# Kernel optimization log

Measured on AMD Instinct MI355X. Metric: run time of the kernel, lower is better.

Reference implementation:

```python
import jax, jax.numpy as jnp
import numpy as np

EPS = 1e-5

def _fake_quant(w, axis):
    # symmetric int8 fake-quant with straight-through estimator
    s = jnp.max(jnp.abs(w), axis=axis, keepdims=True) / 127.0 + 1e-8
    q = jnp.clip(jnp.round(w / s), -127.0, 127.0) * s
    return w + jax.lax.stop_gradient(q - w)

def _qconv1x1(x, w, b):
    # x: [B, C_in, Q, H, W]; w: [C_out, C_in] (1x1 kernel); weight fake-quantized
    wq = _fake_quant(w, axis=1)
    return jnp.einsum('bcqhw,oc->boqhw', x, wq) + b[None, :, None, None, None]

def setup_inputs() -> dict:
    key = jax.random.key(0)
    ks = jax.random.split(key, 12)
    B, C, Q, H, W = 8, 256, 4, 40, 40
    x = jax.random.normal(ks[0], (B, C, Q, H, W), dtype=jnp.float32)
    scale = 1.0 / np.sqrt(C)
    Wq = jax.random.normal(ks[1], (C, C), dtype=jnp.float32) * scale
    Wk = jax.random.normal(ks[2], (C, C), dtype=jnp.float32) * scale
    Wv = jax.random.normal(ks[3], (C, C), dtype=jnp.float32) * scale
    Wp = jax.random.normal(ks[4], (C, C), dtype=jnp.float32) * scale
    bq = jnp.zeros((C,), jnp.float32)
    bk = jnp.zeros((C,), jnp.float32)
    bv = jnp.zeros((C,), jnp.float32)
    bp = jnp.zeros((C,), jnp.float32)
    gamma = jnp.ones((C,), jnp.float32)
    beta = jnp.zeros((C,), jnp.float32)
    return {"x": x, "Wq": Wq, "bq": bq, "Wk": Wk, "bk": bk,
            "Wv": Wv, "bv": bv, "Wp": Wp, "bp": bp,
            "gamma": gamma, "beta": beta}

def reference(x, Wq, bq, Wk, bk, Wv, bv, Wp, bp, gamma, beta):
    B, C, Q, H, W = x.shape
    q = _qconv1x1(x, Wq, bq)
    k = _qconv1x1(x, Wk, bk)
    v = _qconv1x1(x, Wv, bv)
    # per-rotation channel attention: [B, Q=4, C, H*W]
    qh = q.reshape(B, C, Q, H * W).transpose(0, 2, 1, 3)
    kh = k.reshape(B, C, Q, H * W).transpose(0, 2, 1, 3)
    vh = v.reshape(B, C, Q, H * W).transpose(0, 2, 1, 3)
    scale = 1.0 / jnp.sqrt(jnp.float32(C // 4))
    attn = jnp.einsum('bqcn,bqdn->bqcd', qh, kh) * scale  # [B,4,C,C]
    attn = jax.nn.softmax(attn, axis=-1)
    out = jnp.einsum('bqcd,bqdn->bqcn', attn, vh)  # [B,4,C,HW]
    out = out.transpose(0, 2, 1, 3).reshape(B, C, Q, H, W)
    out = _qconv1x1(out, Wp, bp)
    # IQBN: per-channel batchnorm with int8 fake-quantized gamma
    mean = jnp.mean(out, axis=(0, 2, 3, 4), keepdims=True)
    var = jnp.var(out, axis=(0, 2, 3, 4), keepdims=True)
    g = _fake_quant(gamma, axis=None)[None, :, None, None, None]
    b = beta[None, :, None, None, None]
    out = (out - mean) * jax.lax.rsqrt(var + EPS) * g + b
    return out
```

## Files before the change

### kernel.cpp

```cpp
#include <hip/hip_runtime.h>
#include <math.h>

#define BB 8
#define CCH 256
#define QQ 4
#define NN 1600
#define BQN 32
#define SP 51200
#define EPSF 1e-5f

typedef __attribute__((ext_vector_type(8))) short bf16x8;
typedef __attribute__((ext_vector_type(4))) float f32x4;

static __device__ inline ushort f2bf(float f) {
  union { float f; unsigned u; } v; v.f = f;
  return (ushort)((v.u + 0x7fffu + ((v.u >> 16) & 1u)) >> 16);
}
static __device__ inline float bf2f(ushort u) {
  union { unsigned u; float f; } v; v.u = ((unsigned)u) << 16;
  return v.f;
}
static __device__ inline void gld16(const ushort* g, ushort* l) {
  __builtin_amdgcn_global_load_lds(
      (const __attribute__((address_space(1))) unsigned int*)g,
      (__attribute__((address_space(3))) unsigned int*)l, 16, 0, 0);
}

__global__ void quant_weights_kernel(const float* Wq, const float* Wk,
                                     const float* Wv, const float* Wp,
                                     const float* gamma,
                                     ushort* wq, ushort* wk, ushort* wvT, ushort* wp,
                                     ushort* wqT, ushort* wkT, ushort* wpT,
                                     float* gq, float* r, float* d2,
                                     float* m_acc, float* v_acc) {
  __shared__ float red[256];
  int blk = blockIdx.x;
  int tid = threadIdx.x;
  if (blk < 1024) {
    int mat = blk >> 8;
    int row = blk & 255;
    const float* W = (mat == 0) ? Wq : (mat == 1) ? Wk : (mat == 2) ? Wv : Wp;
    float w = W[row * 256 + tid];
    red[tid] = fabsf(w);
    __syncthreads();
    for (int s = 128; s > 0; s >>= 1) {
      if (tid < s) red[tid] = fmaxf(red[tid], red[tid + s]);
      __syncthreads();
    }
    float s = red[0] / 127.0f + 1e-8f;
    float q = fminf(fmaxf(rintf(w / s), -127.0f), 127.0f) * s;
    ushort qb = f2bf(q);
    if (mat == 0)      { wq[row * 256 + tid] = qb; wqT[tid * 256 + row] = qb; }
    else if (mat == 1) { wk[row * 256 + tid] = qb; wkT[tid * 256 + row] = qb; }
    else if (mat == 2) { wvT[tid * 256 + row] = qb; }
    else               { wp[row * 256 + tid] = qb; wpT[tid * 256 + row] = qb; }
  } else {
    float g = gamma[tid];
    red[tid] = fabsf(g);
    __syncthreads();
    for (int s = 128; s > 0; s >>= 1) {
      if (tid < s) red[tid] = fmaxf(red[tid], red[tid + s]);
      __syncthreads();
    }
    float s = red[0] / 127.0f + 1e-8f;
    gq[tid] = fminf(fmaxf(rintf(g / s), -127.0f), 127.0f) * s;
    for (int i = tid; i < BQN * 256; i += 256) { r[i] = 0.f; d2[i] = 0.f; }
    m_acc[tid] = 0.f;
    v_acc[tid] = 0.f;
  }
}

__global__ __launch_bounds__(256)
void prep_kernel(const float* __restrict__ x, ushort* __restrict__ xb,
                 ushort* __restrict__ xT, float* __restrict__ r) {
  int bqi = blockIdx.z, b = bqi >> 2, q = bqi & 3;
  int s0 = blockIdx.x * 64, c0 = blockIdx.y * 64;
  __shared__ ushort lT[64 * 66];
  int tid = threadIdx.x;
  int c = tid >> 2, nch = (tid & 3) * 16;
  const float* xp = x + ((size_t)(b * CCH + c0 + c) * QQ + q) * NN + s0 + nch;
  union { ushort u[16]; int4 v[2]; } nb;
  float s = 0.f;
#pragma unroll
  for (int j = 0; j < 4; j++) {
    float4 f = ((const float4*)xp)[j];
    ushort b0 = f2bf(f.x), b1 = f2bf(f.y), b2 = f2bf(f.z), b3 = f2bf(f.w);
    s += bf2f(b0) + bf2f(b1) + bf2f(b2) + bf2f(b3);
    nb.u[j * 4 + 0] = b0;
    nb.u[j * 4 + 1] = b1;
    nb.u[j * 4 + 2] = b2;
    nb.u[j * 4 + 3] = b3;
    lT[c * 66 + nch + j * 4 + 0] = b0;
    lT[c * 66 + nch + j * 4 + 1] = b1;
    lT[c * 66 + nch + j * 4 + 2] = b2;
    lT[c * 66 + nch + j * 4 + 3] = b3;
  }
  ushort* xbp = xb + (size_t)bqi * (CCH * NN) + (size_t)(c0 + c) * NN + s0 + nch;
  *(int4*)xbp = nb.v[0];
  *((int4*)xbp + 1) = nb.v[1];
  s += __shfl_down(s, 2);
  s += __shfl_down(s, 1);
  if ((tid & 3) == 0) atomicAdd(&r[bqi * 256 + c0 + c], s);
  __syncthreads();
  int n = tid >> 2, cch = (tid & 3) * 16;
  union { ushort u[16]; int4 v[2]; } o;
#pragma unroll
  for (int i = 0; i < 16; i++) o.u[i] = lT[(cch + i) * 66 + n];
  ushort* dst = xT + (size_t)(bqi * NN + s0 + n) * CCH + c0 + cch;
  *(int4*)dst = o.v[0];
  *((int4*)dst + 1) = o.v[1];
}

__global__ __launch_bounds__(256)
void gram_sym_kernel(const ushort* __restrict__ xb, ushort* __restrict__ Gh,
                     ushort* __restrict__ Gl) {
  __shared__ __align__(16) char smem[16384];
  int t = blockIdx.x, z = blockIdx.y;
  int ty = (t >= 4) + (t >= 7) + (t >= 9);
  int base = ty * 4 - (ty * (ty - 1)) / 2;
  int tx = ty + (t - base);
  int mBase = ty * 64, nBase = tx * 64;
  bool offd = (tx != ty);
  int tid = threadIdx.x, wave = tid >> 6, lane = tid & 63;
  int wm = wave >> 1, wn = wave & 1;
  int col = lane & 15, quad = lane >> 4;
  const ushort* X = xb + (size_t)z * (CCH * NN);
  const ushort* gA = X + (size_t)(mBase + (tid >> 2)) * NN + (tid & 3) * 8;
  const ushort* gB = X + (size_t)(nBase + (tid >> 2)) * NN + (tid & 3) * 8;
  f32x4 acc[2][2];
#pragma unroll
  for (int i = 0; i < 2; i++)
#pragma unroll
    for (int j = 0; j < 2; j++) acc[i][j] = (f32x4){0.f, 0.f, 0.f, 0.f};

  const int nIter = NN / 32;
  gld16(gA, (ushort*)smem + tid * 8);
  gld16(gB, (ushort*)(smem + 4096) + tid * 8);
  for (int it = 0; it < nIter; ++it) {
    int cur = it & 1;
    __syncthreads();
    if (it + 1 < nIter) {
      int kt = (it + 1) << 5;
      char* bb = smem + (cur ^ 1) * 8192;
      gld16(gA + kt, (ushort*)bb + tid * 8);
      gld16(gB + kt, (ushort*)(bb + 4096) + tid * 8);
    }
    const ushort* lA = (const ushort*)(smem + cur * 8192);
    const ushort* lB = lA + 2048;
    bf16x8 af[2], bfr[2];
#pragma unroll
    for (int i = 0; i < 2; i++)
      af[i] = *(const bf16x8*)&lA[(wm * 32 + i * 16 + col) * 32 + quad * 8];
#pragma unroll
    for (int j = 0; j < 2; j++)
      bfr[j] = *(const bf16x8*)&lB[(wn * 32 + j * 16 + col) * 32 + quad * 8];
#pragma unroll
    for (int i = 0; i < 2; i++)
#pragma unroll
      for (int j = 0; j < 2; j++)
        acc[i][j] = __builtin_amdgcn_mfma_f32_16x16x32_bf16(af[i], bfr[j], acc[i][j], 0, 0, 0);
  }
  __syncthreads();
  float* lCw = (float*)smem + wave * 576;
#pragma unroll
  for (int i = 0; i < 2; i++) {
#pragma unroll
    for (int j = 0; j < 2; j++)
#pragma unroll
      for (int rg = 0; rg < 4; rg++)
        lCw[(quad * 4 + rg) * 36 + j * 16 + col] = acc[i][j][rg];
    int mrow0 = mBase + wm * 32 + i * 16;
    int nW = nBase + wn * 32;
    int rr = lane >> 2, cc = (lane & 3) * 8;
    union { ushort u[8]; int4 v; } oh, ol;
#pragma unroll
    for (int t8 = 0; t8 < 8; t8++) {
      float vfl = lCw[rr * 36 + cc + t8];
      ushort hh = f2bf(vfl);
      oh.u[t8] = hh;
      ol.u[t8] = f2bf(vfl - bf2f(hh));
    }
    size_t off = (size_t)z * 65536 + (size_t)(mrow0 + rr) * 256 + nW + cc;
    *(int4*)(Gh + off) = oh.v;
    *(int4*)(Gl + off) = ol.v;
    if (offd) {
      int nn = lane >> 1, mh = (lane & 1) * 8;
      union { ushort u[8]; int4 v; } th, tl;
#pragma unroll
      for (int t8 = 0; t8 < 8; t8++) {
        float vfl = lCw[(mh + t8) * 36 + nn];
        ushort hh = f2bf(vfl);
        th.u[t8] = hh;
        tl.u[t8] = f2bf(vfl - bf2f(hh));
      }
      size_t offT = (size_t)z * 65536 + (size_t)(nW + nn) * 256 + mrow0 + mh;
      *(int4*)(Gh + offT) = th.v;
      *(int4*)(Gl + offT) = tl.v;
    }
  }
}

__global__ __launch_bounds__(256)
void spk_kernel(const ushort* __restrict__ wq, const ushort* __restrict__ Gh,
                const ushort* __restrict__ Gl, const ushort* __restrict__ wk,
                const float* __restrict__ ug, const float* __restrict__ vg,
                const float* __restrict__ bqv, const float* __restrict__ bkv,
                const float* __restrict__ bvv,
                ushort* __restrict__ P, float* __restrict__ pb) {
  __shared__ __align__(16) char smem[103424];
  int z = blockIdx.y, mBase = blockIdx.x * 32;
  int tid = threadIdx.x, wave = tid >> 6, lane = tid & 63;
  int col = lane & 15, quad = lane >> 4;
  int rA = tid >> 2, sub = (tid & 3) * 8;
  const ushort* Ghz = Gh + (size_t)z * 65536;
  const ushort* Glz = Gl + (size_t)z * 65536;
  ushort* M1h_l = (ushort*)(smem + 69632);
  ushort* M1l_l = M1h_l + 8448;

  f32x4 acc[2][4];
#pragma unroll
  for (int i = 0; i < 2; i++)
#pragma unroll
    for (int j = 0; j < 4; j++) acc[i][j] = (f32x4){0.f, 0.f, 0.f, 0.f};

  auto s1_load = [&](int buf, int kt) {
    ushort* L = (ushort*)(smem + buf * 34816);
    if (tid < 128)
      gld16(wq + (size_t)(mBase + rA) * 256 + kt + sub, L + tid * 8);
    ushort* Lh = L + 1024;
    ushort* Ll = L + 9216;
#pragma unroll
    for (int q = 0; q < 4; q++) {
      int n = q * 64 + rA;
      gld16(Ghz + (size_t)n * 256 + kt + sub, Lh + (q * 256 + tid) * 8);
      gld16(Glz + (size_t)n * 256 + kt + sub, Ll + (q * 256 + tid) * 8);
    }
  };
  s1_load(0, 0);
  for (int it = 0; it < 8; ++it) {
    int cur = it & 1;
    __syncthreads();
    if (it + 1 < 8) s1_load(cur ^ 1, (it + 1) * 32);
    const ushort* L = (const ushort*)(smem + cur * 34816);
    const ushort* lA = L;
    const ushort* lBh = L + 1024;
    const ushort* lBl = L + 9216;
    bf16x8 af[2], bh[4], bl[4];
#pragma unroll
    for (int i = 0; i < 2; i++)
      af[i] = *(const bf16x8*)&lA[(i * 16 + col) * 32 + quad * 8];
#pragma unroll
    for (int j = 0; j < 4; j++) {
      bh[j] = *(const bf16x8*)&lBh[(wave * 64 + j * 16 + col) * 32 + quad * 8];
      bl[j] = *(const bf16x8*)&lBl[(wave * 64 + j * 16 + col) * 32 + quad * 8];
    }
#pragma unroll
    for (int i = 0; i < 2; i++)
#pragma unroll
      for (int j = 0; j < 4; j++) {
        acc[i][j] = __builtin_amdgcn_mfma_f32_16x16x32_bf16(af[i], bh[j], acc[i][j], 0, 0, 0);
        acc[i][j] = __builtin_amdgcn_mfma_f32_16x16x32_bf16(af[i], bl[j], acc[i][j], 0, 0, 0);
      }
  }
#pragma unroll
  for (int i = 0; i < 2; i++)
#pragma unroll
    for (int j = 0; j < 4; j++)
#pragma unroll
      for (int rg = 0; rg < 4; rg++) {
        int ml = i * 16 + quad * 4 + rg;
        int cg = wave * 64 + j * 16 + col;
        float vfl = acc[i][j][rg];
        ushort hh = f2bf(vfl);
        M1h_l[ml * 264 + cg] = hh;
        M1l_l[ml * 264 + cg] = f2bf(vfl - bf2f(hh));
      }

  f32x4 acc2[2][4];
#pragma unroll
  for (int i = 0; i < 2; i++)
#pragma unroll
    for (int j = 0; j < 4; j++) acc2[i][j] = (f32x4){0.f, 0.f, 0.f, 0.f};
  auto s2_load = [&](int buf, int kt) {
    ushort* L = (ushort*)(smem + buf * 34816);
#pragma unroll
    for (int q = 0; q < 4; q++)
      gld16(wk + (size_t)(q * 64 + rA) * 256 + kt + sub, L + (q * 256 + tid) * 8);
  };
  s2_load(0, 0);
  for (int it = 0; it < 8; ++it) {
    int cur = it & 1;
    __syncthreads();
    if (it + 1 < 8) s2_load(cur ^ 1, (it + 1) * 32);
    const ushort* lB = (const ushort*)(smem + cur * 34816);
    int kt = it * 32;
    bf16x8 ah[2], al[2], bfr[4];
#pragma unroll
    for (int i = 0; i < 2; i++) {
      ah[i] = *(const bf16x8*)&M1h_l[(i * 16 + col) * 264 + kt + quad * 8];
      al[i] = *(const bf16x8*)&M1l_l[(i * 16 + col) * 264 + kt + quad * 8];
    }
#pragma unroll
    for (int j = 0; j < 4; j++)
      bfr[j] = *(const bf16x8*)&lB[(wave * 64 + j * 16 + col) * 32 + quad * 8];
#pragma unroll
    for (int i = 0; i < 2; i++)
#pragma unroll
      for (int j = 0; j < 4; j++) {
        acc2[i][j] = __builtin_amdgcn_mfma_f32_16x16x32_bf16(ah[i], bfr[j], acc2[i][j], 0, 0, 0);
        acc2[i][j] = __builtin_amdgcn_mfma_f32_16x16x32_bf16(al[i], bfr[j], acc2[i][j], 0, 0, 0);
      }
  }
  __syncthreads();

  float* Sb = (float*)(smem + 69632);
  float bkc[4], vvc[4];
#pragma unroll
  for (int j = 0; j < 4; j++) {
    int cg = wave * 64 + j * 16 + col;
    bkc[j] = bkv[cg];
    vvc[j] = vg[z * 256 + cg];
  }
#pragma unroll
  for (int i = 0; i < 2; i++)
#pragma unroll
    for (int rg = 0; rg < 4; rg++) {
      int ml = i * 16 + quad * 4 + rg;
      int rglob = mBase + ml;
      float uu = ug[z * 256 + rglob];
      float bqc = bqv[rglob];
#pragma unroll
      for (int j = 0; j < 4; j++)
        Sb[ml * 260 + wave * 64 + j * 16 + col] =
            0.125f * (acc2[i][j][rg] + uu * bkc[j] + bqc * vvc[j] + 1600.0f * bqc * bkc[j]);
    }
  __syncthreads();

  float4 bv4 = *(const float4*)(bvv + lane * 4);
#pragma unroll
  for (int rr8 = 0; rr8 < 8; ++rr8) {
    int rloc = wave * 8 + rr8;
    f32x4 sv = *(const f32x4*)&Sb[rloc * 260 + lane * 4];
    float x0 = sv[0], x1 = sv[1], x2 = sv[2], x3 = sv[3];
    float m = fmaxf(fmaxf(x0, x1), fmaxf(x2, x3));
#pragma unroll
    for (int s = 32; s > 0; s >>= 1) m = fmaxf(m, __shfl_xor(m, s));
    float e0 = expf(x0 - m), e1 = expf(x1 - m), e2 = expf(x2 - m), e3 = expf(x3 - m);
    float t = e0 + e1 + e2 + e3;
#pragma unroll
    for (int s = 32; s > 0; s >>= 1) t += __shfl_xor(t, s);
    float is = 1.0f / t;
    float p0 = e0 * is, p1 = e1 * is, p2 = e2 * is, p3 = e3 * is;
    union { ushort u[4]; uint2 v; } o;
    o.u[0] = f2bf(p0); o.u[1] = f2bf(p1); o.u[2] = f2bf(p2); o.u[3] = f2bf(p3);
    *(uint2*)(P + (size_t)z * 65536 + (size_t)(mBase + rloc) * 256 + lane * 4) = o.v;
    float d = p0 * bv4.x + p1 * bv4.y + p2 * bv4.z + p3 * bv4.w;
#pragma unroll
    for (int s = 32; s > 0; s >>= 1) d += __shfl_xor(d, s);
    if (lane == 0) pb[z * 256 + mBase + rloc] = d;
  }
}

__global__ __launch_bounds__(256)
void pt_kernel(const ushort* __restrict__ P, const ushort* __restrict__ wvT,
               const ushort* __restrict__ wp,
               ushort* __restrict__ Tm, ushort* __restrict__ TmT) {
  __shared__ __align__(16) char smem[53760];
  int z = blockIdx.y, cs = blockIdx.x * 32;
  int tid = threadIdx.x, wave = tid >> 6, lane = tid & 63;
  int col = lane & 15, quad = lane >> 4;
  int rA = tid >> 2, sub = (tid & 3) * 8;
  const ushort* Pz = P + (size_t)z * 65536;
  ushort* N1b = (ushort*)(smem + 36864);

  f32x4 acc[4][2];
#pragma unroll
  for (int i = 0; i < 4; i++)
#pragma unroll
    for (int j = 0; j < 2; j++) acc[i][j] = (f32x4){0.f, 0.f, 0.f, 0.f};
  auto s3_load = [&](int buf, int kt) {
    ushort* L = (ushort*)(smem + buf * 18432);
#pragma unroll
    for (int q = 0; q < 4; q++)
      gld16(Pz + (size_t)(q * 64 + rA) * 256 + kt + sub, L + (q * 256 + tid) * 8);
    if (tid < 128)
      gld16(wvT + (size_t)(cs + rA) * 256 + kt + sub, L + 8192 + tid * 8);
  };
  s3_load(0, 0);
  for (int it = 0; it < 8; ++it) {
    int cur = it & 1;
    __syncthreads();
    if (it + 1 < 8) s3_load(cur ^ 1, (it + 1) * 32);
    const ushort* lP = (const ushort*)(smem + cur * 18432);
    const ushort* lV = lP + 8192;
    bf16x8 af[4], bfr[2];
#pragma unroll
    for (int i = 0; i < 4; i++)
      af[i] = *(const bf16x8*)&lP[(wave * 64 + i * 16 + col) * 32 + quad * 8];
#pragma unroll
    for (int j = 0; j < 2; j++)
      bfr[j] = *(const bf16x8*)&lV[(j * 16 + col) * 32 + quad * 8];
#pragma unroll
    for (int i = 0; i < 4; i++)
#pragma unroll
      for (int j = 0; j < 2; j++)
        acc[i][j] = __builtin_amdgcn_mfma_f32_16x16x32_bf16(af[i], bfr[j], acc[i][j], 0, 0, 0);
  }
#pragma unroll
  for (int i = 0; i < 4; i++)
#pragma unroll
    for (int j = 0; j < 2; j++)
#pragma unroll
      for (int rg = 0; rg < 4; rg++) {
        int e = wave * 64 + i * 16 + quad * 4 + rg;
        int cl = j * 16 + col;
        N1b[cl * 264 + e] = f2bf(acc[i][j][rg]);
      }

  f32x4 acc2[4][2];
#pragma unroll
  for (int i = 0; i < 4; i++)
#pragma unroll
    for (int j = 0; j < 2; j++) acc2[i][j] = (f32x4){0.f, 0.f, 0.f, 0.f};
  auto s4_load = [&](int buf, int kt) {
    ushort* L = (ushort*)(smem + buf * 18432);
#pragma unroll
    for (int q = 0; q < 4; q++)
      gld16(wp + (size_t)(q * 64 + rA) * 256 + kt + sub, L + (q * 256 + tid) * 8);
  };
  s4_load(0, 0);
  for (int it = 0; it < 8; ++it) {
    int cur = it & 1;
    __syncthreads();
    if (it + 1 < 8) s4_load(cur ^ 1, (it + 1) * 32);
    const ushort* lW = (const ushort*)(smem + cur * 18432);
    int kt = it * 32;
    bf16x8 af[4], bfr[2];
#pragma unroll
    for (int i = 0; i < 4; i++)
      af[i] = *(const bf16x8*)&lW[(wave * 64 + i * 16 + col) * 32 + quad * 8];
#pragma unroll
    for (int j = 0; j < 2; j++)
      bfr[j] = *(const bf16x8*)&N1b[(j * 16 + col) * 264 + kt + quad * 8];
#pragma unroll
    for (int i = 0; i < 4; i++)
#pragma unroll
      for (int j = 0; j < 2; j++)
        acc2[i][j] = __builtin_amdgcn_mfma_f32_16x16x32_bf16(af[i], bfr[j], acc2[i][j], 0, 0, 0);
  }
  __syncthreads();
  float* lCw = (float*)smem + wave * 576;
#pragma unroll
  for (int i = 0; i < 4; i++) {
#pragma unroll
    for (int j = 0; j < 2; j++)
#pragma unroll
      for (int rg = 0; rg < 4; rg++)
        lCw[(quad * 4 + rg) * 36 + j * 16 + col] = acc2[i][j][rg];
    int oW = wave * 64 + i * 16;
    int rr = lane >> 2, cc = (lane & 3) * 8;
    union { ushort u[8]; int4 v; } o;
#pragma unroll
    for (int t8 = 0; t8 < 8; t8++) o.u[t8] = f2bf(lCw[rr * 36 + cc + t8]);
    *(int4*)(Tm + (size_t)z * 65536 + (size_t)(oW + rr) * 256 + cs + cc) = o.v;
    int nn = lane >> 1, mh = (lane & 1) * 8;
    union { ushort u[8]; int4 v; } o2;
#pragma unroll
    for (int t8 = 0; t8 < 8; t8++) o2.u[t8] = f2bf(lCw[(mh + t8) * 36 + nn]);
    *(int4*)(TmT + (size_t)z * 65536 + (size_t)(cs + nn) * 256 + oW + mh) = o2.v;
  }
}

template<int MODE>
__global__ __launch_bounds__(256)
void gemm64(const ushort* __restrict__ A, long sA, const ushort* __restrict__ A2,
            const ushort* __restrict__ B, long sB, const ushort* __restrict__ B2,
            void* __restrict__ C1, void* __restrict__ C2, long sC) {
  constexpr bool SPB = (MODE == 0 || MODE == 4);
  constexpr bool SPA = (MODE == 1);
  constexpr int BUFB = (SPA || SPB) ? 12288 : 8192;
  __shared__ __align__(16) char smem[2 * BUFB];
  int z = blockIdx.z;
  int mBase = blockIdx.y * 64, nBase = blockIdx.x * 64;
  int tid = threadIdx.x, wave = tid >> 6, lane = tid & 63;
  int wm = wave >> 1, wn = wave & 1;
  int col = lane & 15, quad = lane >> 4;
  const ushort* gA = A + (size_t)z * sA + (size_t)(mBase + (tid >> 2)) * 256 + (tid & 3) * 8;
  const ushort* gB = B + (size_t)z * sB + (size_t)(nBase + (tid >> 2)) * 256 + (tid & 3) * 8;
  const ushort* gX = nullptr;
  if (SPB) gX = B2 + (size_t)z * sB + (size_t)(nBase + (tid >> 2)) * 256 + (tid & 3) * 8;
  if (SPA) gX = A2 + (size_t)z * sA + (size_t)(mBase + (tid >> 2)) * 256 + (tid & 3) * 8;

  f32x4 acc[2][2];
#pragma unroll
  for (int i = 0; i < 2; i++)
#pragma unroll
    for (int j = 0; j < 2; j++) acc[i][j] = (f32x4){0.f, 0.f, 0.f, 0.f};

  {
    char* bb = smem;
    gld16(gA, (ushort*)bb + tid * 8);
    gld16(gB, (ushort*)(bb + 4096) + tid * 8);
    if (SPA || SPB) gld16(gX, (ushort*)(bb + 8192) + tid * 8);
  }
  for (int it = 0; it < 8; ++it) {
    int cur = it & 1;
    __syncthreads();
    if (it + 1 < 8) {
      int kt = (it + 1) * 32;
      char* bb = smem + (cur ^ 1) * BUFB;
      gld16(gA + kt, (ushort*)bb + tid * 8);
      gld16(gB + kt, (ushort*)(bb + 4096) + tid * 8);
      if (SPA || SPB) gld16(gX + kt, (ushort*)(bb + 8192) + tid * 8);
    }
    const ushort* lA = (const ushort*)(smem + cur * BUFB);
    const ushort* lB = lA + 2048;
    const ushort* lX = lA + 4096;
    bf16x8 af[2], bfv[2], xf[2];
#pragma unroll
    for (int i = 0; i < 2; i++)
      af[i] = *(const bf16x8*)&lA[(wm * 32 + i * 16 + col) * 32 + quad * 8];
#pragma unroll
    for (int j = 0; j < 2; j++)
      bfv[j] = *(const bf16x8*)&lB[(wn * 32 + j * 16 + col) * 32 + quad * 8];
    if (SPB) {
#pragma unroll
      for (int j = 0; j < 2; j++)
        xf[j] = *(const bf16x8*)&lX[(wn * 32 + j * 16 + col) * 32 + quad * 8];
    } else if (SPA) {
#pragma unroll
      for (int i = 0; i < 2; i++)
        xf[i] = *(const bf16x8*)&lX[(wm * 32 + i * 16 + col) * 32 + quad * 8];
    }
#pragma unroll
    for (int i = 0; i < 2; i++)
#pragma unroll
      for (int j = 0; j < 2; j++) {
        acc[i][j] = __builtin_amdgcn_mfma_f32_16x16x32_bf16(af[i], bfv[j], acc[i][j], 0, 0, 0);
        if (SPB)
          acc[i][j] = __builtin_amdgcn_mfma_f32_16x16x32_bf16(af[i], xf[j], acc[i][j], 0, 0, 0);
        if (SPA)
          acc[i][j] = __builtin_amdgcn_mfma_f32_16x16x32_bf16(xf[i], bfv[j], acc[i][j], 0, 0, 0);
      }
  }

  if (MODE == 4) {
    const ushort* Tz = A + (size_t)z * sA;
    float* d2 = (float*)C1;
#pragma unroll
    for (int i = 0; i < 2; i++) {
      int mr = mBase + wm * 32 + i * 16 + quad * 4;
#pragma unroll
      for (int rg = 0; rg < 4; rg++) {
        float p = 0.f;
#pragma unroll
        for (int j = 0; j < 2; j++)
          p += acc[i][j][rg] * bf2f(Tz[(mr + rg) * 256 + nBase + wn * 32 + j * 16 + col]);
        p += __shfl_down(p, 8);
        p += __shfl_down(p, 4);
        p += __shfl_down(p, 2);
        p += __shfl_down(p, 1);
        if (col == 0) atomicAdd(d2 + z * 256 + mr + rg, p);
      }
    }
    return;
  }
}

__global__ __launch_bounds__(256)
void uv_kernel(const ushort* __restrict__ wqT, const ushort* __restrict__ wkT,
               const float* __restrict__ r, float* __restrict__ u,
               float* __restrict__ vv) {
  int bq = blockIdx.x, sel = blockIdx.y, c = threadIdx.x;
  __shared__ float rs[256];
  rs[c] = r[bq * 256 + c];
  __syncthreads();
  const ushort* WT = sel ? wkT : wqT;
  float s = 0.f;
  for (int i = 0; i < 256; i++) s += bf2f(WT[i * 256 + c]) * rs[i];
  (sel ? vv : u)[bq * 256 + c] = s;
}

__global__ __launch_bounds__(256)
void bo_d1_kernel(const ushort* __restrict__ wpT, const ushort* __restrict__ TmT,
                  const float* __restrict__ pb, const float* __restrict__ rb,
                  const float* __restrict__ bp, const float* __restrict__ d2,
                  float* __restrict__ bo, float* __restrict__ m_acc,
                  float* __restrict__ v_acc) {
  int z = blockIdx.x, o = threadIdx.x;
  __shared__ float sp[256], sr[256];
  sp[o] = pb[z * 256 + o];
  sr[o] = rb[z * 256 + o];
  __syncthreads();
  float bv = bp[o], d1 = 0.f;
  const ushort* Tz = TmT + (size_t)z * 65536;
  for (int c = 0; c < 256; c++) {
    bv += bf2f(wpT[c * 256 + o]) * sp[c];
    d1 += bf2f(Tz[c * 256 + o]) * sr[c];
  }
  bo[z * 256 + o] = bv;
  atomicAdd(m_acc + o, d1 + 1600.0f * bv);
  atomicAdd(v_acc + o, d2[z * 256 + o] + 2.0f * bv * d1 + 1600.0f * bv * bv);
}

__global__ __launch_bounds__(256)
void final_kernel(const ushort* __restrict__ Tm, const ushort* __restrict__ xT,
                  const float* __restrict__ bo, const float* __restrict__ m_acc,
                  const float* __restrict__ v_acc, const float* __restrict__ gq,
                  const float* __restrict__ beta, float* __restrict__ out) {
  __shared__ __align__(16) char smem[32768];
  float* lC = (float*)smem;
  int z = blockIdx.z;
  int mBase = blockIdx.y * 128, nBase = blockIdx.x * 128;
  int tid = threadIdx.x, wave = tid >> 6, lane = tid & 63;
  int wm = wave >> 1, wn = wave & 1;
  int col = lane & 15, quad = lane >> 4;
  int srow = tid >> 2, skc = (tid & 3) * 8;
  const ushort* Az = Tm + (size_t)z * 65536;
  const ushort* Bz = xT + (size_t)z * (NN * 256);
  const ushort* gA  = Az + (size_t)(mBase + srow) * 256 + skc;
  const ushort* gA2 = gA + 64 * 256;
  int br1 = nBase + srow;      br1 = br1 < NN ? br1 : NN - 1;
  int br2 = nBase + 64 + srow; br2 = br2 < NN ? br2 : NN - 1;
  const ushort* gB  = Bz + (size_t)br1 * 256 + skc;
  const ushort* gB2 = Bz + (size_t)br2 * 256 + skc;
  ushort* sA1[2]; ushort* sA2[2]; ushort* sB1[2]; ushort* sB2[2];
#pragma unroll
  for (int b = 0; b < 2; b++) {
    ushort* lAb = (ushort*)(smem + b * 16384);
    ushort* lBb = (ushort*)(smem + b * 16384 + 8192);
    sA1[b] = &lAb[srow * 32 + skc];
    sA2[b] = &lAb[(64 + srow) * 32 + skc];
    sB1[b] = &lBb[srow * 32 + skc];
    sB2[b] = &lBb[(64 + srow) * 32 + skc];
  }
  f32x4 acc[4][4];
#pragma unroll
  for (int i = 0; i < 4; i++)
#pragma unroll
    for (int j = 0; j < 4; j++) acc[i][j] = (f32x4){0.f, 0.f, 0.f, 0.f};

  const int nIter = 8;
  gld16(gA, sA1[0]); gld16(gA2, sA2[0]); gld16(gB, sB1[0]); gld16(gB2, sB2[0]);
  for (int it = 0; it < nIter; ++it) {
    int cur = it & 1;
    __syncthreads();
    if (it + 1 < nIter) {
      int kt = (it + 1) << 5, nxt = cur ^ 1;
      gld16(gA + kt, sA1[nxt]); gld16(gA2 + kt, sA2[nxt]);
      gld16(gB + kt, sB1[nxt]); gld16(gB2 + kt, sB2[nxt]);
    }
    const ushort* lAc = (const ushort*)(smem + cur * 16384);
    const ushort* lBc = (const ushort*)(smem + cur * 16384 + 8192);
    bf16x8 af[4], bfr[4];
#pragma unroll
    for (int i = 0; i < 4; i++)
      af[i] = *(const bf16x8*)&lAc[(wm * 64 + i * 16 + col) * 32 + quad * 8];
#pragma unroll
    for (int j = 0; j < 4; j++)
      bfr[j] = *(const bf16x8*)&lBc[(wn * 64 + j * 16 + col) * 32 + quad * 8];
#pragma unroll
    for (int i = 0; i < 4; i++)
#pragma unroll
      for (int j = 0; j < 4; j++)
        acc[i][j] = __builtin_amdgcn_mfma_f32_16x16x32_bf16(af[i], bfr[j], acc[i][j], 0, 0, 0);
  }
  __syncthreads();
  float* lCw = lC + wave * 16 * 68;
  int mW = mBase + wm * 64, nW = nBase + wn * 64;
  int b = z >> 2, q = z & 3;
  const float inv = 1.0f / (float)SP;
#pragma unroll
  for (int i = 0; i < 4; i++) {
#pragma unroll
    for (int j = 0; j < 4; j++)
#pragma unroll
      for (int rg = 0; rg < 4; rg++)
        lCw[(quad * 4 + rg) * 68 + j * 16 + col] = acc[i][j][rg];
    int mrow0 = mW + i * 16;
    int rr = lane & 15, cc = lane >> 4;
    int n0 = nW + cc * 16;
    int o = mrow0 + rr;
    float bi = bo[(size_t)z * 256 + o];
    float mean = m_acc[o] * inv;
    float var = v_acc[o] * inv - mean * mean;
    float scl = rsqrtf(var + EPSF) * gq[o];
    float be = beta[o];
    if (n0 < NN) {
      float* C = out + (size_t)b * (CCH * QQ * NN)
               + (size_t)o * (QQ * NN) + (size_t)q * NN + n0;
#pragma unroll
      for (int v = 0; v < 4; v++) {
        float4 f;
        f.x = (lCw[rr * 68 + cc * 16 + v * 4 + 0] + bi - mean) * scl + be;
        f.y = (lCw[rr * 68 + cc * 16 + v * 4 + 1] + bi - mean) * scl + be;
        f.z = (lCw[rr * 68 + cc * 16 + v * 4 + 2] + bi - mean) * scl + be;
        f.w = (lCw[rr * 68 + cc * 16 + v * 4 + 3] + bi - mean) * scl + be;
        *(float4*)(C + v * 4) = f;
      }
    }
  }
}

extern "C" void kernel_launch(void* const* d_in, const int* in_sizes, int n_in,
                              void* d_out, int out_size, void* d_ws, size_t ws_size,
                              hipStream_t stream) {
  const float* x     = (const float*)d_in[0];
  const float* Wq    = (const float*)d_in[1];
  const float* bq    = (const float*)d_in[2];
  const float* Wk    = (const float*)d_in[3];
  const float* bk    = (const float*)d_in[4];
  const float* Wv    = (const float*)d_in[5];
  const float* bv    = (const float*)d_in[6];
  const float* Wp    = (const float*)d_in[7];
  const float* bp    = (const float*)d_in[8];
  const float* gamma = (const float*)d_in[9];
  const float* beta  = (const float*)d_in[10];
  float* out = (float*)d_out;

  ushort* h    = (ushort*)d_ws;
  ushort* wq   = h;
  ushort* wk   = wq + 65536;
  ushort* wp   = wk + 65536;
  ushort* wvT  = wp + 65536;
  ushort* wqT  = wvT + 65536;
  ushort* wkT  = wqT + 65536;
  ushort* wpT  = wkT + 65536;
  ushort* xb   = wpT + 65536;
  ushort* xT   = xb + (size_t)BQN * CCH * NN;
  ushort* Gh   = xT + (size_t)BQN * CCH * NN;
  ushort* Gl   = Gh + (size_t)BQN * 65536;
  ushort* P    = Gl + (size_t)BQN * 65536;
  ushort* Tm   = P + (size_t)BQN * 65536;
  ushort* TmT  = Tm + (size_t)BQN * 65536;
  float*  r    = (float*)(TmT + (size_t)BQN * 65536);
  float*  u    = r + 8192;
  float*  vv   = u + 8192;
  float*  pb   = vv + 8192;
  float*  bo   = pb + 8192;
  float*  d2   = bo + 8192;
  float*  m_acc = d2 + 8192;
  float*  v_acc = m_acc + 256;
  float*  gq   = v_acc + 256;

  quant_weights_kernel<<<1025, 256, 0, stream>>>(Wq, Wk, Wv, Wp, gamma,
                                                 wq, wk, wvT, wp, wqT, wkT, wpT,
                                                 gq, r, d2, m_acc, v_acc);
  prep_kernel<<<dim3(NN / 64, CCH / 64, BQN), 256, 0, stream>>>(x, xb, xT, r);
  uv_kernel<<<dim3(BQN, 2), 256, 0, stream>>>(wqT, wkT, r, u, vv);
  gram_sym_kernel<<<dim3(10, BQN), 256, 0, stream>>>(xb, Gh, Gl);
  spk_kernel<<<dim3(8, BQN), 256, 0, stream>>>(wq, Gh, Gl, wk, u, vv, bq, bk, bv, P, pb);
  pt_kernel<<<dim3(8, BQN), 256, 0, stream>>>(P, wvT, wp, Tm, TmT);
  gemm64<4><<<dim3(4, 4, BQN), 256, 0, stream>>>(
      Tm, 65536, nullptr, Gh, 65536, Gl, d2, nullptr, 0);
  bo_d1_kernel<<<BQN, 256, 0, stream>>>(wpT, TmT, pb, r, bp, d2, bo, m_acc, v_acc);
  final_kernel<<<dim3(13, 2, BQN), 256, 0, stream>>>(Tm, xT, bo, m_acc, v_acc,
                                                     gq, beta, out);
}
```

Before: 250.9 us.

## Merge weight quant with x prep, fold uv into gram, fuse d2 with bo

Merges the weight-quantization and x-preparation kernels into one launch, replacing atomic row-sum accumulation with per-tile partial sums written to a buffer. The uv projection is folded into the gram kernel as an extra block column that first reduces those partial sums. The d2 GEMM and the bo/d1 kernel become one launch that atomically accumulates straight into v_acc, and m_acc/v_acc zeroing moves into pt_kernel. Going from nine launches to six cuts launch gaps and atomic traffic, but the fused variance accumulation depends on launch ordering and adds extra blocks whose work is imbalanced.

```diff
diff --git a/kernel.cpp b/kernel.cpp
--- a/kernel.cpp
+++ b/kernel.cpp
@@ -26,14 +26,18 @@
       (__attribute__((address_space(3))) unsigned int*)l, 16, 0, 0);
 }
 
-__global__ void quant_weights_kernel(const float* Wq, const float* Wk,
-                                     const float* Wv, const float* Wp,
-                                     const float* gamma,
-                                     ushort* wq, ushort* wk, ushort* wvT, ushort* wp,
-                                     ushort* wqT, ushort* wkT, ushort* wpT,
-                                     float* gq, float* r, float* d2,
-                                     float* m_acc, float* v_acc) {
+__global__ __launch_bounds__(256)
+void qp_kernel(const float* __restrict__ Wq, const float* __restrict__ Wk,
+               const float* __restrict__ Wv, const float* __restrict__ Wp,
+               const float* __restrict__ gamma, const float* __restrict__ x,
+               ushort* __restrict__ wq, ushort* __restrict__ wk,
+               ushort* __restrict__ wvT, ushort* __restrict__ wp,
+               ushort* __restrict__ wqT, ushort* __restrict__ wkT,
+               ushort* __restrict__ wpT, float* __restrict__ gq,
+               ushort* __restrict__ xb, ushort* __restrict__ xT,
+               float* __restrict__ rpart) {
   __shared__ float red[256];
+  __shared__ ushort lT[64 * 66];
   int blk = blockIdx.x;
   int tid = threadIdx.x;
   if (blk < 1024) {
@@ -54,7 +58,9 @@
     else if (mat == 1) { wk[row * 256 + tid] = qb; wkT[tid * 256 + row] = qb; }
     else if (mat == 2) { wvT[tid * 256 + row] = qb; }
     else               { wp[row * 256 + tid] = qb; wpT[tid * 256 + row] = qb; }
-  } else {
+    return;
+  }
+  if (blk == 1024) {
     float g = gamma[tid];
     red[tid] = fabsf(g);
     __syncthreads();
@@ -64,19 +70,14 @@
     }
     float s = red[0] / 127.0f + 1e-8f;
     gq[tid] = fminf(fmaxf(rintf(g / s), -127.0f), 127.0f) * s;
-    for (int i = tid; i < BQN * 256; i += 256) { r[i] = 0.f; d2[i] = 0.f; }
-    m_acc[tid] = 0.f;
-    v_acc[tid] = 0.f;
-  }
-}
-
-__global__ __launch_bounds__(256)
-void prep_kernel(const float* __restrict__ x, ushort* __restrict__ xb,
-                 ushort* __restrict__ xT, float* __restrict__ r) {
-  int bqi = blockIdx.z, b = bqi >> 2, q = bqi & 3;
-  int s0 = blockIdx.x * 64, c0 = blockIdx.y * 64;
-  __shared__ ushort lT[64 * 66];
-  int tid = threadIdx.x;
+    return;
+  }
+  int p = blk - 1025;
+  int sx = p % 25;
+  int rem = p / 25;
+  int cy = rem & 3, bqi = rem >> 2;
+  int b = bqi >> 2, q = bqi & 3;
+  int s0 = sx * 64, c0 = cy * 64;
   int c = tid >> 2, nch = (tid & 3) * 16;
   const float* xp = x + ((size_t)(b * CCH + c0 + c) * QQ + q) * NN + s0 + nch;
   union { ushort u[16]; int4 v[2]; } nb;
@@ -100,7 +101,7 @@
   *((int4*)xbp + 1) = nb.v[1];
   s += __shfl_down(s, 2);
   s += __shfl_down(s, 1);
-  if ((tid & 3) == 0) atomicAdd(&r[bqi * 256 + c0 + c], s);
+  if ((tid & 3) == 0) rpart[((size_t)bqi * 25 + sx) * 256 + c0 + c] = s;
   __syncthreads();
   int n = tid >> 2, cch = (tid & 3) * 16;
   union { ushort u[16]; int4 v[2]; } o;
@@ -112,16 +113,38 @@
 }
 
 __global__ __launch_bounds__(256)
-void gram_sym_kernel(const ushort* __restrict__ xb, ushort* __restrict__ Gh,
-                     ushort* __restrict__ Gl) {
+void gram_uv_kernel(const ushort* __restrict__ xb, ushort* __restrict__ Gh,
+                    ushort* __restrict__ Gl,
+                    const ushort* __restrict__ wqT, const ushort* __restrict__ wkT,
+                    const float* __restrict__ rpart, float* __restrict__ r,
+                    float* __restrict__ u, float* __restrict__ vv) {
   __shared__ __align__(16) char smem[16384];
+  __shared__ float rs[256];
   int t = blockIdx.x, z = blockIdx.y;
+  int tid = threadIdx.x;
+  if (t == 10) {
+    float rv = 0.f;
+#pragma unroll
+    for (int k = 0; k < 25; k++) rv += rpart[((size_t)z * 25 + k) * 256 + tid];
+    rs[tid] = rv;
+    r[z * 256 + tid] = rv;
+    __syncthreads();
+    float su = 0.f, sv = 0.f;
+    for (int i = 0; i < 256; i++) {
+      float rr = rs[i];
+      su += bf2f(wqT[i * 256 + tid]) * rr;
+      sv += bf2f(wkT[i * 256 + tid]) * rr;
+    }
+    u[z * 256 + tid] = su;
+    vv[z * 256 + tid] = sv;
+    return;
+  }
   int ty = (t >= 4) + (t >= 7) + (t >= 9);
   int base = ty * 4 - (ty * (ty - 1)) / 2;
   int tx = ty + (t - base);
   int mBase = ty * 64, nBase = tx * 64;
   bool offd = (tx != ty);
-  int tid = threadIdx.x, wave = tid >> 6, lane = tid & 63;
+  int wave = tid >> 6, lane = tid & 63;
   int wm = wave >> 1, wn = wave & 1;
   int col = lane & 15, quad = lane >> 4;
   const ushort* X = xb + (size_t)z * (CCH * NN);
@@ -364,12 +387,17 @@
 __global__ __launch_bounds__(256)
 void pt_kernel(const ushort* __restrict__ P, const ushort* __restrict__ wvT,
                const ushort* __restrict__ wp,
-               ushort* __restrict__ Tm, ushort* __restrict__ TmT) {
+               ushort* __restrict__ Tm, ushort* __restrict__ TmT,
+               float* __restrict__ m_acc, float* __restrict__ v_acc) {
   __shared__ __align__(16) char smem[53760];
   int z = blockIdx.y, cs = blockIdx.x * 32;
   int tid = threadIdx.x, wave = tid >> 6, lane = tid & 63;
   int col = lane & 15, quad = lane >> 4;
   int rA = tid >> 2, sub = (tid & 3) * 8;
+  if (blockIdx.x == 0 && blockIdx.y == 0) {
+    m_acc[tid] = 0.f;
+    v_acc[tid] = 0.f;
+  }
   const ushort* Pz = P + (size_t)z * 65536;
   ushort* N1b = (ushort*)(smem + 36864);
 
@@ -471,25 +499,44 @@
   }
 }
 
-template<int MODE>
 __global__ __launch_bounds__(256)
-void gemm64(const ushort* __restrict__ A, long sA, const ushort* __restrict__ A2,
-            const ushort* __restrict__ B, long sB, const ushort* __restrict__ B2,
-            void* __restrict__ C1, void* __restrict__ C2, long sC) {
-  constexpr bool SPB = (MODE == 0 || MODE == 4);
-  constexpr bool SPA = (MODE == 1);
-  constexpr int BUFB = (SPA || SPB) ? 12288 : 8192;
-  __shared__ __align__(16) char smem[2 * BUFB];
-  int z = blockIdx.z;
-  int mBase = blockIdx.y * 64, nBase = blockIdx.x * 64;
-  int tid = threadIdx.x, wave = tid >> 6, lane = tid & 63;
+void dsq_bo_kernel(const ushort* __restrict__ Tm, const ushort* __restrict__ Gh,
+                   const ushort* __restrict__ Gl,
+                   const ushort* __restrict__ wpT, const ushort* __restrict__ TmT,
+                   const float* __restrict__ pb, const float* __restrict__ rb,
+                   const float* __restrict__ bp, float* __restrict__ bo,
+                   float* __restrict__ m_acc, float* __restrict__ v_acc) {
+  __shared__ __align__(16) char smem[24576];
+  int blk = blockIdx.x;
+  int tid = threadIdx.x;
+  if (blk >= 512) {
+    int z = blk - 512;
+    float* sp = (float*)smem;
+    float* sr = sp + 256;
+    sp[tid] = pb[z * 256 + tid];
+    sr[tid] = rb[z * 256 + tid];
+    __syncthreads();
+    float bv = bp[tid], d1 = 0.f;
+    const ushort* Tz = TmT + (size_t)z * 65536;
+    for (int c = 0; c < 256; c++) {
+      bv += bf2f(wpT[c * 256 + tid]) * sp[c];
+      d1 += bf2f(Tz[c * 256 + tid]) * sr[c];
+    }
+    bo[z * 256 + tid] = bv;
+    atomicAdd(m_acc + tid, d1 + 1600.0f * bv);
+    atomicAdd(v_acc + tid, 2.0f * bv * d1 + 1600.0f * bv * bv);
+    return;
+  }
+  int z = blk >> 4;
+  int mBase = ((blk >> 2) & 3) * 64, nBase = (blk & 3) * 64;
+  int wave = tid >> 6, lane = tid & 63;
   int wm = wave >> 1, wn = wave & 1;
   int col = lane & 15, quad = lane >> 4;
-  const ushort* gA = A + (size_t)z * sA + (size_t)(mBase + (tid >> 2)) * 256 + (tid & 3) * 8;
-  const ushort* gB = B + (size_t)z * sB + (size_t)(nBase + (tid >> 2)) * 256 + (tid & 3) * 8;
-  const ushort* gX = nullptr;
-  if (SPB) gX = B2 + (size_t)z * sB + (size_t)(nBase + (tid >> 2)) * 256 + (tid & 3) * 8;
-  if (SPA) gX = A2 + (size_t)z * sA + (size_t)(mBase + (tid >> 2)) * 256 + (tid & 3) * 8;
+  int srow = tid >> 2, skc = (tid & 3) * 8;
+  const ushort* Tz = Tm + (size_t)z * 65536;
+  const ushort* gA = Tz + (size_t)(mBase + srow) * 256 + skc;
+  const ushort* gB = Gh + (size_t)z * 65536 + (size_t)(nBase + srow) * 256 + skc;
+  const ushort* gX = Gl + (size_t)z * 65536 + (size_t)(nBase + srow) * 256 + skc;
 
   f32x4 acc[2][2];
 #pragma unroll
@@ -501,19 +548,19 @@
     char* bb = smem;
     gld16(gA, (ushort*)bb + tid * 8);
     gld16(gB, (ushort*)(bb + 4096) + tid * 8);
-    if (SPA || SPB) gld16(gX, (ushort*)(bb + 8192) + tid * 8);
+    gld16(gX, (ushort*)(bb + 8192) + tid * 8);
   }
   for (int it = 0; it < 8; ++it) {
     int cur = it & 1;
     __syncthreads();
     if (it + 1 < 8) {
       int kt = (it + 1) * 32;
-      char* bb = smem + (cur ^ 1) * BUFB;
+      char* bb = smem + (cur ^ 1) * 12288;
       gld16(gA + kt, (ushort*)bb + tid * 8);
       gld16(gB + kt, (ushort*)(bb + 4096) + tid * 8);
-      if (SPA || SPB) gld16(gX + kt, (ushort*)(bb + 8192) + tid * 8);
-    }
-    const ushort* lA = (const ushort*)(smem + cur * BUFB);
+      gld16(gX + kt, (ushort*)(bb + 8192) + tid * 8);
+    }
+    const ushort* lA = (const ushort*)(smem + cur * 12288);
     const ushort* lB = lA + 2048;
     const ushort* lX = lA + 4096;
     bf16x8 af[2], bfv[2], xf[2];
@@ -521,86 +568,34 @@
     for (int i = 0; i < 2; i++)
       af[i] = *(const bf16x8*)&lA[(wm * 32 + i * 16 + col) * 32 + quad * 8];
 #pragma unroll
-    for (int j = 0; j < 2; j++)
+    for (int j = 0; j < 2; j++) {
       bfv[j] = *(const bf16x8*)&lB[(wn * 32 + j * 16 + col) * 32 + quad * 8];
-    if (SPB) {
-#pragma unroll
-      for (int j = 0; j < 2; j++)
-        xf[j] = *(const bf16x8*)&lX[(wn * 32 + j * 16 + col) * 32 + quad * 8];
-    } else if (SPA) {
-#pragma unroll
-      for (int i = 0; i < 2; i++)
-        xf[i] = *(const bf16x8*)&lX[(wm * 32 + i * 16 + col) * 32 + quad * 8];
+      xf[j]  = *(const bf16x8*)&lX[(wn * 32 + j * 16 + col) * 32 + quad * 8];
     }
 #pragma unroll
     for (int i = 0; i < 2; i++)
 #pragma unroll
       for (int j = 0; j < 2; j++) {
         acc[i][j] = __builtin_amdgcn_mfma_f32_16x16x32_bf16(af[i], bfv[j], acc[i][j], 0, 0, 0);
-        if (SPB)
-          acc[i][j] = __builtin_amdgcn_mfma_f32_16x16x32_bf16(af[i], xf[j], acc[i][j], 0, 0, 0);
-        if (SPA)
-          acc[i][j] = __builtin_amdgcn_mfma_f32_16x16x32_bf16(xf[i], bfv[j], acc[i][j], 0, 0, 0);
+        acc[i][j] = __builtin_amdgcn_mfma_f32_16x16x32_bf16(af[i], xf[j], acc[i][j], 0, 0, 0);
       }
   }
-
-  if (MODE == 4) {
-    const ushort* Tz = A + (size_t)z * sA;
-    float* d2 = (float*)C1;
-#pragma unroll
-    for (int i = 0; i < 2; i++) {
-      int mr = mBase + wm * 32 + i * 16 + quad * 4;
-#pragma unroll
-      for (int rg = 0; rg < 4; rg++) {
-        float p = 0.f;
-#pragma unroll
-        for (int j = 0; j < 2; j++)
-          p += acc[i][j][rg] * bf2f(Tz[(mr + rg) * 256 + nBase + wn * 32 + j * 16 + col]);
-        p += __shfl_down(p, 8);
-        p += __shfl_down(p, 4);
-        p += __shfl_down(p, 2);
-        p += __shfl_down(p, 1);
-        if (col == 0) atomicAdd(d2 + z * 256 + mr + rg, p);
-      }
-    }
-    return;
-  }
-}
-
-__global__ __launch_bounds__(256)
-void uv_kernel(const ushort* __restrict__ wqT, const ushort* __restrict__ wkT,
-               const float* __restrict__ r, float* __restrict__ u,
-               float* __restrict__ vv) {
-  int bq = blockIdx.x, sel = blockIdx.y, c = threadIdx.x;
-  __shared__ float rs[256];
-  rs[c] = r[bq * 256 + c];
-  __syncthreads();
-  const ushort* WT = sel ? wkT : wqT;
-  float s = 0.f;
-  for (int i = 0; i < 256; i++) s += bf2f(WT[i * 256 + c]) * rs[i];
-  (sel ? vv : u)[bq * 256 + c] = s;
-}
-
-__global__ __launch_bounds__(256)
-void bo_d1_kernel(const ushort* __restrict__ wpT, const ushort* __restrict__ TmT,
-                  const float* __restrict__ pb, const float* __restrict__ rb,
-                  const float* __restrict__ bp, const float* __restrict__ d2,
-                  float* __restrict__ bo, float* __restrict__ m_acc,
-                  float* __restrict__ v_acc) {
-  int z = blockIdx.x, o = threadIdx.x;
-  __shared__ float sp[256], sr[256];
-  sp[o] = pb[z * 256 + o];
-  sr[o] = rb[z * 256 + o];
-  __syncthreads();
-  float bv = bp[o], d1 = 0.f;
-  const ushort* Tz = TmT + (size_t)z * 65536;
-  for (int c = 0; c < 256; c++) {
-    bv += bf2f(wpT[c * 256 + o]) * sp[c];
-    d1 += bf2f(Tz[c * 256 + o]) * sr[c];
-  }
-  bo[z * 256 + o] = bv;
-  atomicAdd(m_acc + o, d1 + 1600.0f * bv);
-  atomicAdd(v_acc + o, d2[z * 256 + o] + 2.0f * bv * d1 + 1600.0f * bv * bv);
+#pragma unroll
+  for (int i = 0; i < 2; i++) {
+    int mr = mBase + wm * 32 + i * 16 + quad * 4;
+#pragma unroll
+    for (int rg = 0; rg < 4; rg++) {
+      float p = 0.f;
+#pragma unroll
+      for (int j = 0; j < 2; j++)
+        p += acc[i][j][rg] * bf2f(Tz[(mr + rg) * 256 + nBase + wn * 32 + j * 16 + col]);
+      p += __shfl_down(p, 8);
+      p += __shfl_down(p, 4);
+      p += __shfl_down(p, 2);
+      p += __shfl_down(p, 1);
+      if (col == 0) atomicAdd(v_acc + mr + rg, p);
+    }
+  }
 }
 
 __global__ __launch_bounds__(256)
@@ -738,22 +733,20 @@
   float*  vv   = u + 8192;
   float*  pb   = vv + 8192;
   float*  bo   = pb + 8192;
-  float*  d2   = bo + 8192;
-  float*  m_acc = d2 + 8192;
+  float*  m_acc = bo + 8192;
   float*  v_acc = m_acc + 256;
   float*  gq   = v_acc + 256;
-
-  quant_weights_kernel<<<1025, 256, 0, stream>>>(Wq, Wk, Wv, Wp, gamma,
-                                                 wq, wk, wvT, wp, wqT, wkT, wpT,
-                                                 gq, r, d2, m_acc, v_acc);
-  prep_kernel<<<dim3(NN / 64, CCH / 64, BQN), 256, 0, stream>>>(x, xb, xT, r);
-  uv_kernel<<<dim3(BQN, 2), 256, 0, stream>>>(wqT, wkT, r, u, vv);
-  gram_sym_kernel<<<dim3(10, BQN), 256, 0, stream>>>(xb, Gh, Gl);
+  float*  rpart = gq + 256;
+
+  qp_kernel<<<4225, 256, 0, stream>>>(Wq, Wk, Wv, Wp, gamma, x,
+                                      wq, wk, wvT, wp, wqT, wkT, wpT, gq,
+                                      xb, xT, rpart);
+  gram_uv_kernel<<<dim3(11, BQN), 256, 0, stream>>>(xb, Gh, Gl, wqT, wkT,
+                                                    rpart, r, u, vv);
   spk_kernel<<<dim3(8, BQN), 256, 0, stream>>>(wq, Gh, Gl, wk, u, vv, bq, bk, bv, P, pb);
-  pt_kernel<<<dim3(8, BQN), 256, 0, stream>>>(P, wvT, wp, Tm, TmT);
-  gemm64<4><<<dim3(4, 4, BQN), 256, 0, stream>>>(
-      Tm, 65536, nullptr, Gh, 65536, Gl, d2, nullptr, 0);
-  bo_d1_kernel<<<BQN, 256, 0, stream>>>(wpT, TmT, pb, r, bp, d2, bo, m_acc, v_acc);
+  pt_kernel<<<dim3(8, BQN), 256, 0, stream>>>(P, wvT, wp, Tm, TmT, m_acc, v_acc);
+  dsq_bo_kernel<<<544, 256, 0, stream>>>(Tm, Gh, Gl, wpT, TmT, pb, r, bp,
+                                         bo, m_acc, v_acc);
   final_kernel<<<dim3(13, 2, BQN), 256, 0, stream>>>(Tm, xT, bo, m_acc, v_acc,
                                                      gq, beta, out);
 }
```

Result: no change. 254.6 us (+1.5%).
